# Kernel optimization log

Measured on AMD Instinct MI355X. Metric: run time of the kernel, lower is better.

Reference implementation:

```python
import jax, jax.numpy as jnp
import numpy as np

B = 8192        # batch of spots
T = 137         # target_length: number of predict heads
D = 384         # fea_size(256) + img_size(128)
K = 128         # hidden width of each head
EPS = 1e-5      # BatchNorm1d eps
SLOPE = 0.01    # LeakyReLU negative slope (torch default)


def setup_inputs() -> dict:
    key = jax.random.key(0)
    ks = jax.random.split(key, 5)
    return {
        "f":        jax.random.normal(ks[0], (B, D), dtype=jnp.float32),
        "W1":       jax.random.normal(ks[1], (T, K, D), dtype=jnp.float32) * (1.0 / np.sqrt(D)),
        "b1":       jax.random.normal(ks[2], (T, K), dtype=jnp.float32) * 0.02,
        "gamma":    jnp.ones((T, K), dtype=jnp.float32),
        "beta":     jnp.zeros((T, K), dtype=jnp.float32),
        "run_mean": jnp.zeros((T, K), dtype=jnp.float32),
        "run_var":  jnp.ones((T, K), dtype=jnp.float32),
        "W2":       jax.random.normal(ks[3], (T, K), dtype=jnp.float32) * (1.0 / np.sqrt(K)),
        "b2":       jax.random.normal(ks[4], (T,), dtype=jnp.float32) * 0.02,
    }


def reference(f, W1, b1, gamma, beta, run_mean, run_var, W2, b2):
    # Batched equivalent of: for i in range(137): Linear(384->128)+BN+LeakyReLU+Linear(128->1)
    # all applied to the same feature f; outputs concatenated -> [B, 137].
    h = jnp.einsum('bd,tkd->btk', f, W1) + b1                       # [B, T, K]
    scale = gamma * jax.lax.rsqrt(run_var + EPS)                     # eval-mode BN, [T, K]
    h = (h - run_mean) * scale + beta
    h = jnp.where(h >= 0, h, SLOPE * h)                              # LeakyReLU
    out = jnp.einsum('btk,tk->bt', h, W2) + b2                       # [B, T]
    return out
```

## Files before the change

### kernel.cpp

```cpp
#include <hip/hip_runtime.h>
#include <hip/hip_bf16.h>

constexpr int BATCH = 8192;
constexpr int THEADS = 137;
constexpr int DFEA = 384;
constexpr int KHID = 128;
constexpr float EPS_BN = 1e-5f;
constexpr float SLOPE = 0.01f;

constexpr size_t N_F  = (size_t)BATCH * DFEA;
constexpr size_t N_W1 = (size_t)THEADS * KHID * DFEA;
constexpr size_t WS_NEED = (N_F + N_W1) * sizeof(__hip_bfloat16);
constexpr int C_F8 = (int)(N_F / 8);
constexpr int C_T8 = (int)((N_F + N_W1) / 8);

typedef __attribute__((ext_vector_type(8))) short bf16x8;
typedef __attribute__((ext_vector_type(4))) float f32x4;

__device__ __forceinline__ short cvt_bf16(float x) {
    __hip_bfloat16 b = __float2bfloat16(x);
    return *(short*)&b;
}

__device__ __forceinline__ bf16x8 load8_cvt(const float* __restrict__ g) {
    f32x4 lo = *(const f32x4*)g;
    f32x4 hi = *(const f32x4*)(g + 4);
    bf16x8 r;
    r[0] = cvt_bf16(lo[0]); r[1] = cvt_bf16(lo[1]);
    r[2] = cvt_bf16(lo[2]); r[3] = cvt_bf16(lo[3]);
    r[4] = cvt_bf16(hi[0]); r[5] = cvt_bf16(hi[1]);
    r[6] = cvt_bf16(hi[2]); r[7] = cvt_bf16(hi[3]);
    return r;
}

__device__ __forceinline__ void gload16(const void* g, void* s) {
    __builtin_amdgcn_global_load_lds((const __attribute__((address_space(1))) void*)g,
                                     (__attribute__((address_space(3))) void*)s,
                                     16, 0, 0);
}

__global__ __launch_bounds__(256) void cvt_pass(const float* __restrict__ f,
                                                const float* __restrict__ W1,
                                                __hip_bfloat16* __restrict__ ws) {
    int i = blockIdx.x * 256 + threadIdx.x;
    if (i < C_F8)
        *(bf16x8*)(ws + (size_t)i * 8) = load8_cvt(f + (size_t)i * 8);
    else if (i < C_T8)
        *(bf16x8*)(ws + (size_t)i * 8) = load8_cvt(W1 + ((size_t)i - C_F8) * 8);
}

__global__ __launch_bounds__(256, 2) void fused_heads_v5(
    const __hip_bfloat16* __restrict__ fb,
    const __hip_bfloat16* __restrict__ W1b,
    const float* __restrict__ b1,
    const float* __restrict__ gmm,
    const float* __restrict__ bta,
    const float* __restrict__ rmean,
    const float* __restrict__ rvar,
    const float* __restrict__ W2,
    const float* __restrict__ b2,
    float* __restrict__ out)
{
    __shared__ __attribute__((aligned(16))) __hip_bfloat16 As[2][256 * 32];
    __shared__ __attribute__((aligned(16))) __hip_bfloat16 Bs[2][128 * 32];

    const int tid  = threadIdx.x;
    const int lane = tid & 63;
    const int wm   = tid >> 6;
    const int m0 = blockIdx.x * 256;
    const int t  = blockIdx.y;
    const int n0 = t * KHID;

    const int row16 = lane & 15;
    const int quad  = lane >> 4;
    const int swz   = quad ^ ((row16 >> 1) & 3);

    const __hip_bfloat16* gA[4];
    const __hip_bfloat16* gB[2];
    #pragma unroll
    for (int c = 0; c < 4; ++c) {
        const int li = tid + c * 256;
        const int r = li >> 2, cb = (li & 3) ^ ((li >> 3) & 3);
        gA[c] = fb + (size_t)(m0 + r) * DFEA + cb * 8;
    }
    #pragma unroll
    for (int c = 0; c < 2; ++c) {
        const int li = tid + c * 256;
        const int r = li >> 2, cb = (li & 3) ^ ((li >> 3) & 3);
        gB[c] = W1b + (size_t)(n0 + r) * DFEA + cb * 8;
    }

    f32x4 acc[4][8];
    #pragma unroll
    for (int i = 0; i < 4; ++i)
        #pragma unroll
        for (int j = 0; j < 8; ++j)
            acc[i][j] = (f32x4){0.f, 0.f, 0.f, 0.f};

#define STAGE(BUF, K0)                                                      \
    {                                                                       \
        _Pragma("unroll")                                                   \
        for (int c = 0; c < 4; ++c)                                         \
            gload16(gA[c] + (K0), &As[BUF][(tid + c * 256) * 8]);           \
        _Pragma("unroll")                                                   \
        for (int c = 0; c < 2; ++c)                                         \
            gload16(gB[c] + (K0), &Bs[BUF][(tid + c * 256) * 8]);           \
    }

    STAGE(0, 0);

    #pragma unroll 2
    for (int kt = 0; kt < DFEA / 32; ++kt) {
        const int cur = kt & 1;
        if (kt < 11) {
            STAGE(cur ^ 1, (kt + 1) * 32);
            asm volatile("s_waitcnt vmcnt(6)" ::: "memory");
        } else {
            asm volatile("s_waitcnt vmcnt(0)" ::: "memory");
        }
        __builtin_amdgcn_s_barrier();
        __builtin_amdgcn_sched_barrier(0);

        bf16x8 af[4], bfr[8];
        #pragma unroll
        for (int ai = 0; ai < 4; ++ai)
            af[ai] = *(const bf16x8*)&As[cur][(wm * 64 + ai * 16 + row16) * 32 + swz * 8];
        #pragma unroll
        for (int bi = 0; bi < 8; ++bi)
            bfr[bi] = *(const bf16x8*)&Bs[cur][(bi * 16 + row16) * 32 + swz * 8];

        __builtin_amdgcn_s_setprio(1);
        #pragma unroll
        for (int ai = 0; ai < 4; ++ai)
            #pragma unroll
            for (int bi = 0; bi < 8; ++bi)
                acc[ai][bi] = __builtin_amdgcn_mfma_f32_16x16x32_bf16(
                    af[ai], bfr[bi], acc[ai][bi], 0, 0, 0);
        __builtin_amdgcn_s_setprio(0);

        __builtin_amdgcn_s_barrier();
    }
#undef STAGE

    float s[8], cc[8], w2v[8];
    #pragma unroll
    for (int bi = 0; bi < 8; ++bi) {
        const int n = n0 + bi * 16 + row16;
        const float sv = gmm[n] * rsqrtf(rvar[n] + EPS_BN);
        s[bi]   = sv;
        cc[bi]  = bta[n] + (b1[n] - rmean[n]) * sv;
        w2v[bi] = W2[n];
    }

    float p[4][4];
    #pragma unroll
    for (int ai = 0; ai < 4; ++ai)
        #pragma unroll
        for (int r = 0; r < 4; ++r) {
            float a = 0.f;
            #pragma unroll
            for (int bi = 0; bi < 8; ++bi) {
                float y = acc[ai][bi][r] * s[bi] + cc[bi];
                y = (y >= 0.f) ? y : SLOPE * y;
                a += y * w2v[bi];
            }
            p[ai][r] = a;
        }

    #pragma unroll
    for (int mask = 1; mask <= 8; mask <<= 1)
        #pragma unroll
        for (int ai = 0; ai < 4; ++ai)
            #pragma unroll
            for (int r = 0; r < 4; ++r)
                p[ai][r] += __shfl_xor(p[ai][r], mask);

    if (row16 == 0) {
        const float bias = b2[t];
        #pragma unroll
        for (int ai = 0; ai < 4; ++ai)
            #pragma unroll
            for (int r = 0; r < 4; ++r) {
                const int row = m0 + wm * 64 + ai * 16 + quad * 4 + r;
                out[(size_t)row * THEADS + t] = p[ai][r] + bias;
            }
    }
}

__global__ __launch_bounds__(256) void fused_heads_f32(
    const float* __restrict__ f, const float* __restrict__ W1,
    const float* __restrict__ b1, const float* __restrict__ gmm,
    const float* __restrict__ bta, const float* __restrict__ rmean,
    const float* __restrict__ rvar, const float* __restrict__ W2,
    const float* __restrict__ b2, float* __restrict__ out)
{
    __shared__ __attribute__((aligned(16))) __hip_bfloat16 As[128 * 32];
    __shared__ __attribute__((aligned(16))) __hip_bfloat16 Bs[128 * 32];
    __shared__ float red[2][128];

    const int tid  = threadIdx.x;
    const int lane = tid & 63;
    const int wave = tid >> 6;
    const int wmv = wave >> 1, wn = wave & 1;
    const int m0 = blockIdx.x * 128;
    const int t  = blockIdx.y;
    const int n0 = t * KHID;

    const int li0 = tid, li1 = tid + 256;
    const int r0 = li0 >> 2, c0 = (li0 & 3) * 8;
    const int r1 = li1 >> 2, c1 = (li1 & 3) * 8;
    const float* gA0 = f  + (size_t)(m0 + r0) * DFEA + c0;
    const float* gA1 = f  + (size_t)(m0 + r1) * DFEA + c1;
    const float* gB0 = W1 + (size_t)(n0 + r0) * DFEA + c0;
    const float* gB1 = W1 + (size_t)(n0 + r1) * DFEA + c1;

    const int row16 = lane & 15, quad = lane >> 4;

    f32x4 acc[4][4];
    #pragma unroll
    for (int i = 0; i < 4; ++i)
        #pragma unroll
        for (int jx = 0; jx < 4; ++jx)
            acc[i][jx] = (f32x4){0.f, 0.f, 0.f, 0.f};

    #pragma unroll 1
    for (int kt = 0; kt < DFEA / 32; ++kt) {
        const int k0 = kt * 32;
        bf16x8 va0 = load8_cvt(gA0 + k0);
        bf16x8 va1 = load8_cvt(gA1 + k0);
        bf16x8 vb0 = load8_cvt(gB0 + k0);
        bf16x8 vb1 = load8_cvt(gB1 + k0);
        __syncthreads();
        *(bf16x8*)&As[li0 * 8] = va0;
        *(bf16x8*)&As[li1 * 8] = va1;
        *(bf16x8*)&Bs[li0 * 8] = vb0;
        *(bf16x8*)&Bs[li1 * 8] = vb1;
        __syncthreads();

        bf16x8 af[4], bfr[4];
        #pragma unroll
        for (int i = 0; i < 4; ++i)
            af[i] = *(const bf16x8*)&As[(wmv * 64 + i * 16 + row16) * 32 + quad * 8];
        #pragma unroll
        for (int i = 0; i < 4; ++i)
            bfr[i] = *(const bf16x8*)&Bs[(wn * 64 + i * 16 + row16) * 32 + quad * 8];
        #pragma unroll
        for (int ai = 0; ai < 4; ++ai)
            #pragma unroll
            for (int bi = 0; bi < 4; ++bi)
                acc[ai][bi] = __builtin_amdgcn_mfma_f32_16x16x32_bf16(
                    af[ai], bfr[bi], acc[ai][bi], 0, 0, 0);
    }

    float s[4], cc[4], w2v[4];
    #pragma unroll
    for (int bi = 0; bi < 4; ++bi) {
        const int n = n0 + wn * 64 + bi * 16 + row16;
        const float sv = gmm[n] * rsqrtf(rvar[n] + EPS_BN);
        s[bi] = sv;
        cc[bi] = bta[n] + (b1[n] - rmean[n]) * sv;
        w2v[bi] = W2[n];
    }
    float p[4][4];
    #pragma unroll
    for (int ai = 0; ai < 4; ++ai)
        #pragma unroll
        for (int r = 0; r < 4; ++r) {
            float a = 0.f;
            #pragma unroll
            for (int bi = 0; bi < 4; ++bi) {
                float y = acc[ai][bi][r] * s[bi] + cc[bi];
                y = (y >= 0.f) ? y : SLOPE * y;
                a += y * w2v[bi];
            }
            p[ai][r] = a;
        }
    #pragma unroll
    for (int mask = 1; mask <= 8; mask <<= 1)
        #pragma unroll
        for (int ai = 0; ai < 4; ++ai)
            #pragma unroll
            for (int r = 0; r < 4; ++r)
                p[ai][r] += __shfl_xor(p[ai][r], mask);
    if (row16 == 0) {
        #pragma unroll
        for (int ai = 0; ai < 4; ++ai)
            #pragma unroll
            for (int r = 0; r < 4; ++r)
                red[wn][wmv * 64 + ai * 16 + quad * 4 + r] = p[ai][r];
    }
    __syncthreads();
    if (tid < 128)
        out[(size_t)(m0 + tid) * THEADS + t] = red[0][tid] + red[1][tid] + b2[t];
}

extern "C" void kernel_launch(void* const* d_in, const int* in_sizes, int n_in,
                              void* d_out, int out_size, void* d_ws, size_t ws_size,
                              hipStream_t stream) {
    (void)in_sizes; (void)n_in; (void)out_size;
    const float* f     = (const float*)d_in[0];
    const float* W1    = (const float*)d_in[1];
    const float* b1    = (const float*)d_in[2];
    const float* gmm   = (const float*)d_in[3];
    const float* bta   = (const float*)d_in[4];
    const float* rmean = (const float*)d_in[5];
    const float* rvar  = (const float*)d_in[6];
    const float* W2    = (const float*)d_in[7];
    const float* b2    = (const float*)d_in[8];
    float* out = (float*)d_out;

    if (ws_size >= WS_NEED) {
        __hip_bfloat16* fb  = (__hip_bfloat16*)d_ws;
        __hip_bfloat16* W1b = fb + N_F;
        cvt_pass<<<(C_T8 + 255) / 256, 256, 0, stream>>>(f, W1, fb);
        dim3 grid(BATCH / 256, THEADS);
        fused_heads_v5<<<grid, 256, 0, stream>>>(fb, W1b, b1, gmm, bta, rmean, rvar, W2, b2, out);
    } else {
        dim3 grid(BATCH / 128, THEADS);
        fused_heads_f32<<<grid, 256, 0, stream>>>(f, W1, b1, gmm, bta, rmean, rvar, W2, b2, out);
    }
}
```

Before: 223.1 us.

## Triple-buffer LDS staging with one barrier per k-step

Switches the GEMM mainloop from double to triple LDS buffering. Two k-tiles are prefetched ahead, and each k-step now has a single barrier where there were two. The aim is to hide more global-load latency and cut synchronisation overhead. LDS use grows from 48KB to 72KB per block, which could reduce occupancy below the 2-blocks target. The waitcnt of 6 still assumes only one stage is in flight, which may make the wait stricter than needed.

After: 221.5 us. Within noise of the previous version (-0.7%).

```diff
diff --git a/kernel.cpp b/kernel.cpp
--- a/kernel.cpp
+++ b/kernel.cpp
@@ -49,7 +49,7 @@
         *(bf16x8*)(ws + (size_t)i * 8) = load8_cvt(W1 + ((size_t)i - C_F8) * 8);
 }
 
-__global__ __launch_bounds__(256, 2) void fused_heads_v5(
+__global__ __launch_bounds__(256, 2) void fused_heads_v8(
     const __hip_bfloat16* __restrict__ fb,
     const __hip_bfloat16* __restrict__ W1b,
     const float* __restrict__ b1,
@@ -61,8 +61,8 @@
     const float* __restrict__ b2,
     float* __restrict__ out)
 {
-    __shared__ __attribute__((aligned(16))) __hip_bfloat16 As[2][256 * 32];
-    __shared__ __attribute__((aligned(16))) __hip_bfloat16 Bs[2][128 * 32];
+    __shared__ __attribute__((aligned(16))) __hip_bfloat16 As[3][256 * 32];
+    __shared__ __attribute__((aligned(16))) __hip_bfloat16 Bs[3][128 * 32];
 
     const int tid  = threadIdx.x;
     const int lane = tid & 63;
@@ -108,38 +108,39 @@
     }
 
     STAGE(0, 0);
-
-    #pragma unroll 2
-    for (int kt = 0; kt < DFEA / 32; ++kt) {
-        const int cur = kt & 1;
-        if (kt < 11) {
-            STAGE(cur ^ 1, (kt + 1) * 32);
-            asm volatile("s_waitcnt vmcnt(6)" ::: "memory");
-        } else {
-            asm volatile("s_waitcnt vmcnt(0)" ::: "memory");
-        }
-        __builtin_amdgcn_s_barrier();
-        __builtin_amdgcn_sched_barrier(0);
-
-        bf16x8 af[4], bfr[8];
-        #pragma unroll
-        for (int ai = 0; ai < 4; ++ai)
-            af[ai] = *(const bf16x8*)&As[cur][(wm * 64 + ai * 16 + row16) * 32 + swz * 8];
-        #pragma unroll
-        for (int bi = 0; bi < 8; ++bi)
-            bfr[bi] = *(const bf16x8*)&Bs[cur][(bi * 16 + row16) * 32 + swz * 8];
-
-        __builtin_amdgcn_s_setprio(1);
-        #pragma unroll
-        for (int ai = 0; ai < 4; ++ai)
-            #pragma unroll
-            for (int bi = 0; bi < 8; ++bi)
-                acc[ai][bi] = __builtin_amdgcn_mfma_f32_16x16x32_bf16(
-                    af[ai], bfr[bi], acc[ai][bi], 0, 0, 0);
-        __builtin_amdgcn_s_setprio(0);
-
-        __builtin_amdgcn_s_barrier();
-    }
+    STAGE(1, 32);
+
+#define KSTEP(KT, CUR, STG)                                                   \
+    {                                                                         \
+        if ((KT) < 11) { asm volatile("s_waitcnt vmcnt(6)" ::: "memory"); }   \
+        else           { asm volatile("s_waitcnt vmcnt(0)" ::: "memory"); }   \
+        __builtin_amdgcn_s_barrier();            \
+        __builtin_amdgcn_sched_barrier(0);       \
+        if ((KT) < 10) STAGE(STG, ((KT) + 2) * 32);                           \
+        bf16x8 af[4], bfr[8];                                                 \
+        _Pragma("unroll")                                                     \
+        for (int ai = 0; ai < 4; ++ai)                                        \
+            af[ai] = *(const bf16x8*)&As[CUR][(wm * 64 + ai * 16 + row16) * 32 + swz * 8]; \
+        _Pragma("unroll")                                                     \
+        for (int bi = 0; bi < 8; ++bi)                                        \
+            bfr[bi] = *(const bf16x8*)&Bs[CUR][(bi * 16 + row16) * 32 + swz * 8]; \
+        __builtin_amdgcn_s_setprio(1);                                        \
+        _Pragma("unroll")                                                     \
+        for (int ai = 0; ai < 4; ++ai)                                        \
+            _Pragma("unroll")                                                 \
+            for (int bi = 0; bi < 8; ++bi)                                    \
+                acc[ai][bi] = __builtin_amdgcn_mfma_f32_16x16x32_bf16(        \
+                    af[ai], bfr[bi], acc[ai][bi], 0, 0, 0);                   \
+        __builtin_amdgcn_s_setprio(0);                                        \
+    }
+
+    #pragma unroll
+    for (int kp = 0; kp < 4; ++kp) {
+        KSTEP(3 * kp,     0, 2)
+        KSTEP(3 * kp + 1, 1, 0)
+        KSTEP(3 * kp + 2, 2, 1)
+    }
+#undef KSTEP
 #undef STAGE
 
     float s[8], cc[8], w2v[8];
@@ -314,7 +315,7 @@
         __hip_bfloat16* W1b = fb + N_F;
         cvt_pass<<<(C_T8 + 255) / 256, 256, 0, stream>>>(f, W1, fb);
         dim3 grid(BATCH / 256, THEADS);
-        fused_heads_v5<<<grid, 256, 0, stream>>>(fb, W1b, b1, gmm, bta, rmean, rvar, W2, b2, out);
+        fused_heads_v8<<<grid, 256, 0, stream>>>(fb, W1b, b1, gmm, bta, rmean, rvar, W2, b2, out);
     } else {
         dim3 grid(BATCH / 128, THEADS);
         fused_heads_f32<<<grid, 256, 0, stream>>>(f, W1, b1, gmm, bta, rmean, rvar, W2, b2, out);
```
